# Kernel optimization log

Hardware: AMD Instinct MI355X
Metric: run time of the kernel (lower is better)

The kernel has to match this reference:

```python
import jax, jax.numpy as jnp
import numpy as np

B, T, D = 8, 4096, 1024


def setup_inputs() -> dict:
    key = jax.random.key(0)
    k1, k2 = jax.random.split(key)
    x = jax.random.normal(k1, (B, T, D), dtype=jnp.float32)
    lengths = jax.random.randint(k2, (B,), 0, T, dtype=jnp.int64)
    return {"x": x, "lengths": lengths}


def reference(x, lengths):
    # x: [B, T, D]; lengths: [B]
    # Original torch code materializes a [B,T,T,D] tensor via
    # (tril * pairwise_padding_mask)[..., None] * gelu(x)[:, None] and sums over
    # the source axis. Algebraically:
    #   out[b,i] = x[b,i] + m[b,i] * sum_{j<=i} m[b,j] * gelu(x[b,j])
    # where m[b,t] = (t < lengths[b]). This is a masked causal prefix sum.
    t = x.shape[1]
    valid = (jnp.arange(t)[None, :] < lengths[:, None]).astype(x.dtype)  # [B,T]
    g = jax.nn.gelu(x, approximate=False) * valid[:, :, None]           # [B,T,D]
    prefix = jnp.cumsum(g, axis=1)                                      # [B,T,D]
    return x + valid[:, :, None] * prefix
```

## Files before the change

### kernel.cpp

```cpp
#include <hip/hip_runtime.h>
#include <math.h>

#define BB 8
#define TT 4096
#define DD 1024
#define NC 256
#define CT (TT / NC)
#define D4 (DD / 4)

typedef float vfloat4 __attribute__((ext_vector_type(4)));

__device__ __forceinline__ float gelu_exact(float v) {
    return 0.5f * v * (1.0f + erff(v * 0.70710678118654752f));
}

__device__ __forceinline__ void gelu_acc(float4& s, const float4 v) {
    s.x += gelu_exact(v.x);
    s.y += gelu_exact(v.y);
    s.z += gelu_exact(v.z);
    s.w += gelu_exact(v.w);
}

__global__ __launch_bounds__(256)
void k_partial(const float* __restrict__ x, const int* __restrict__ lengths,
               float* __restrict__ ws) {
    const int c  = blockIdx.x;
    const int b  = blockIdx.y;
    const int d4 = threadIdx.x;
    const int len = lengths[b];
    const int t0 = c * CT;
    if (t0 >= len) return;
    const int t1 = min(t0 + CT, len);

    const float4* __restrict__ xp = (const float4*)(x + (size_t)b * TT * DD);
    float4 s = make_float4(0.f, 0.f, 0.f, 0.f);
    #pragma unroll 4
    for (int t = t0; t < t1; ++t) {
        float4 v = xp[(size_t)t * D4 + d4];
        gelu_acc(s, v);
    }
    ((float4*)ws)[((size_t)b * NC + c) * D4 + d4] = s;
}

__global__ __launch_bounds__(256)
void k_apply(const float* __restrict__ x, const int* __restrict__ lengths,
             const float* __restrict__ ws, float* __restrict__ out) {
    const int c  = blockIdx.x;
    const int b  = blockIdx.y;
    const int d4 = threadIdx.x;
    const int len = lengths[b];
    const int t0 = c * CT;
    const int tv = min(t0 + CT, len);

    const float4* __restrict__ xp = (const float4*)(x + (size_t)b * TT * DD);
    vfloat4* __restrict__ op = (vfloat4*)(out + (size_t)b * TT * DD);

    int t = t0;
    if (t0 < len) {
        float4 p0 = make_float4(0.f, 0.f, 0.f, 0.f);
        float4 p1 = make_float4(0.f, 0.f, 0.f, 0.f);
        const float4* __restrict__ aggp =
            (const float4*)ws + (size_t)b * NC * D4 + d4;
        int cc = 0;
        #pragma unroll 4
        for (; cc + 1 < c; cc += 2) {
            float4 a0 = aggp[(size_t)cc * D4];
            float4 a1 = aggp[(size_t)(cc + 1) * D4];
            p0.x += a0.x; p0.y += a0.y; p0.z += a0.z; p0.w += a0.w;
            p1.x += a1.x; p1.y += a1.y; p1.z += a1.z; p1.w += a1.w;
        }
        if (cc < c) {
            float4 a0 = aggp[(size_t)cc * D4];
            p0.x += a0.x; p0.y += a0.y; p0.z += a0.z; p0.w += a0.w;
        }
        float4 pre = make_float4(p0.x + p1.x, p0.y + p1.y,
                                 p0.z + p1.z, p0.w + p1.w);

        #pragma unroll 4
        for (; t < tv; ++t) {
            float4 v = xp[(size_t)t * D4 + d4];
            gelu_acc(pre, v);
            vfloat4 o = {v.x + pre.x, v.y + pre.y, v.z + pre.z, v.w + pre.w};
            __builtin_nontemporal_store(o, &op[(size_t)t * D4 + d4]);
        }
    }
    #pragma unroll 4
    for (; t < t0 + CT; ++t) {
        float4 v = xp[(size_t)t * D4 + d4];
        vfloat4 o = {v.x, v.y, v.z, v.w};
        __builtin_nontemporal_store(o, &op[(size_t)t * D4 + d4]);
    }
}

extern "C" void kernel_launch(void* const* d_in, const int* in_sizes, int n_in,
                              void* d_out, int out_size, void* d_ws, size_t ws_size,
                              hipStream_t stream) {
    const float* x       = (const float*)d_in[0];
    const int*   lengths = (const int*)d_in[1];
    float*       out     = (float*)d_out;
    float*       ws      = (float*)d_ws;

    dim3 blk(256, 1, 1);
    dim3 g1(NC, BB, 1);
    hipLaunchKernelGGL(k_partial, g1, blk, 0, stream, x, lengths, ws);
    hipLaunchKernelGGL(k_apply,   g1, blk, 0, stream, x, lengths, ws, out);
}
```

Measured before the change: 267.2 us.

## Add hierarchical super-chunk prefix pass to cut per-block aggregate summation

Adds a middle kernel that sums chunk aggregates into super-chunk prefixes, one for every 16 chunks. The apply kernel then starts from the stored super-chunk prefix and adds at most 15 chunk aggregates, instead of re-summing up to 255 for each block. This removes quadratic re-reading of the workspace aggregates. The partial kernel now writes zero aggregates for chunks past the length, so the new prefixes stay correct. In exchange it adds a third kernel launch and one more dependency between stages.

```diff
diff --git a/kernel.cpp b/kernel.cpp
--- a/kernel.cpp
+++ b/kernel.cpp
@@ -7,6 +7,11 @@
 #define NC 256
 #define CT (TT / NC)
 #define D4 (DD / 4)
+#define SCW 16
+#define SC (NC / SCW)
+
+#define AGG_OFF 0
+#define PFX_OFF (BB * NC * DD)
 
 typedef float vfloat4 __attribute__((ext_vector_type(4)));
 
@@ -21,6 +26,10 @@
     s.w += gelu_exact(v.w);
 }
 
+__device__ __forceinline__ void f4_acc(float4& s, const float4 a) {
+    s.x += a.x; s.y += a.y; s.z += a.z; s.w += a.w;
+}
+
 __global__ __launch_bounds__(256)
 void k_partial(const float* __restrict__ x, const int* __restrict__ lengths,
                float* __restrict__ ws) {
@@ -29,7 +38,6 @@
     const int d4 = threadIdx.x;
     const int len = lengths[b];
     const int t0 = c * CT;
-    if (t0 >= len) return;
     const int t1 = min(t0 + CT, len);
 
     const float4* __restrict__ xp = (const float4*)(x + (size_t)b * TT * DD);
@@ -39,7 +47,31 @@
         float4 v = xp[(size_t)t * D4 + d4];
         gelu_acc(s, v);
     }
-    ((float4*)ws)[((size_t)b * NC + c) * D4 + d4] = s;
+    ((float4*)(ws + AGG_OFF))[((size_t)b * NC + c) * D4 + d4] = s;
+}
+
+__global__ __launch_bounds__(256)
+void k_sprefix(float* __restrict__ ws) {
+    const int s  = blockIdx.x;
+    const int b  = blockIdx.y;
+    const int d4 = threadIdx.x;
+    const int n  = s * SCW;
+
+    const float4* __restrict__ aggp =
+        (const float4*)(ws + AGG_OFF) + (size_t)b * NC * D4 + d4;
+    float4 p0 = make_float4(0.f, 0.f, 0.f, 0.f);
+    float4 p1 = make_float4(0.f, 0.f, 0.f, 0.f);
+    int cc = 0;
+    #pragma unroll 4
+    for (; cc + 1 < n; cc += 2) {
+        float4 a0 = aggp[(size_t)cc * D4];
+        float4 a1 = aggp[(size_t)(cc + 1) * D4];
+        f4_acc(p0, a0);
+        f4_acc(p1, a1);
+    }
+    if (cc < n) f4_acc(p0, aggp[(size_t)cc * D4]);
+    f4_acc(p0, p1);
+    ((float4*)(ws + PFX_OFF))[((size_t)b * SC + s) * D4 + d4] = p0;
 }
 
 __global__ __launch_bounds__(256)
@@ -57,24 +89,23 @@
 
     int t = t0;
     if (t0 < len) {
-        float4 p0 = make_float4(0.f, 0.f, 0.f, 0.f);
+        const int sc = c / SCW;
+        float4 pre =
+            ((const float4*)(ws + PFX_OFF))[((size_t)b * SC + sc) * D4 + d4];
+
+        const float4* __restrict__ aggp =
+            (const float4*)(ws + AGG_OFF) + (size_t)b * NC * D4 + d4;
         float4 p1 = make_float4(0.f, 0.f, 0.f, 0.f);
-        const float4* __restrict__ aggp =
-            (const float4*)ws + (size_t)b * NC * D4 + d4;
-        int cc = 0;
+        int cc = sc * SCW;
         #pragma unroll 4
         for (; cc + 1 < c; cc += 2) {
             float4 a0 = aggp[(size_t)cc * D4];
             float4 a1 = aggp[(size_t)(cc + 1) * D4];
-            p0.x += a0.x; p0.y += a0.y; p0.z += a0.z; p0.w += a0.w;
-            p1.x += a1.x; p1.y += a1.y; p1.z += a1.z; p1.w += a1.w;
+            f4_acc(pre, a0);
+            f4_acc(p1, a1);
         }
-        if (cc < c) {
-            float4 a0 = aggp[(size_t)cc * D4];
-            p0.x += a0.x; p0.y += a0.y; p0.z += a0.z; p0.w += a0.w;
-        }
-        float4 pre = make_float4(p0.x + p1.x, p0.y + p1.y,
-                                 p0.z + p1.z, p0.w + p1.w);
+        if (cc < c) f4_acc(pre, aggp[(size_t)cc * D4]);
+        f4_acc(pre, p1);
 
         #pragma unroll 4
         for (; t < tv; ++t) {
@@ -103,5 +134,9 @@
     dim3 blk(256, 1, 1);
     dim3 g1(NC, BB, 1);
     hipLaunchKernelGGL(k_partial, g1, blk, 0, stream, x, lengths, ws);
-    hipLaunchKernelGGL(k_apply,   g1, blk, 0, stream, x, lengths, ws, out);
+
+    dim3 g15(SC, BB, 1);
+    hipLaunchKernelGGL(k_sprefix, g15, blk, 0, stream, ws);
+
+    hipLaunchKernelGGL(k_apply, g1, blk, 0, stream, x, lengths, ws, out);
 }
```

After: 275.2 us. +3.0%, slower.

## Fuse partial and apply kernels into one pass with decoupled chunk flags

Applied to the files above, without the earlier changes.

Merges the two-kernel chunked prefix scan into a single kernel. Each block takes a chunk index from an atomic ticket, computes its chunk's GELU sum, publishes it with a release flag, then spin-waits until all earlier chunks of its batch are flagged before summing their aggregates and writing output. This removes the second kernel launch and the extra pass between launches, and the chunk's x rows may still be in cache when re-read. In exchange it adds a memset of the control area, atomics and spin-waiting, and blocks whose predecessors are slow will stall.

```diff
diff --git a/kernel.cpp b/kernel.cpp
--- a/kernel.cpp
+++ b/kernel.cpp
@@ -7,6 +7,9 @@
 #define NC 256
 #define CT (TT / NC)
 #define D4 (DD / 4)
+
+#define AGG_OFF 0
+#define CTL_OFF (BB * NC * DD)
 
 typedef float vfloat4 __attribute__((ext_vector_type(4)));
 
@@ -21,60 +24,83 @@
     s.w += gelu_exact(v.w);
 }
 
-__global__ __launch_bounds__(256)
-void k_partial(const float* __restrict__ x, const int* __restrict__ lengths,
-               float* __restrict__ ws) {
-    const int c  = blockIdx.x;
-    const int b  = blockIdx.y;
-    const int d4 = threadIdx.x;
-    const int len = lengths[b];
-    const int t0 = c * CT;
-    if (t0 >= len) return;
-    const int t1 = min(t0 + CT, len);
-
-    const float4* __restrict__ xp = (const float4*)(x + (size_t)b * TT * DD);
-    float4 s = make_float4(0.f, 0.f, 0.f, 0.f);
-    #pragma unroll 4
-    for (int t = t0; t < t1; ++t) {
-        float4 v = xp[(size_t)t * D4 + d4];
-        gelu_acc(s, v);
-    }
-    ((float4*)ws)[((size_t)b * NC + c) * D4 + d4] = s;
+__device__ __forceinline__ void f4_acc(float4& s, const float4 a) {
+    s.x += a.x; s.y += a.y; s.z += a.z; s.w += a.w;
 }
 
 __global__ __launch_bounds__(256)
-void k_apply(const float* __restrict__ x, const int* __restrict__ lengths,
-             const float* __restrict__ ws, float* __restrict__ out) {
-    const int c  = blockIdx.x;
-    const int b  = blockIdx.y;
-    const int d4 = threadIdx.x;
+void k_onepass(const float* __restrict__ x, const int* __restrict__ lengths,
+               float* __restrict__ ws, float* __restrict__ out) {
+    float* agg    = ws + AGG_OFF;
+    int*   flags  = (int*)(ws + CTL_OFF);
+    int*   ticket = flags + BB * NC;
+
+    __shared__ int s_tk;
+    __shared__ int s_nr;
+    if (threadIdx.x == 0)
+        s_tk = __hip_atomic_fetch_add(ticket, 1, __ATOMIC_RELAXED,
+                                      __HIP_MEMORY_SCOPE_AGENT);
+    __syncthreads();
+    const int tk  = s_tk;
+    const int b   = tk >> 8;
+    const int c   = tk & (NC - 1);
+    const int d4  = threadIdx.x;
     const int len = lengths[b];
-    const int t0 = c * CT;
-    const int tv = min(t0 + CT, len);
+    const int t0  = c * CT;
+    const int tv  = min(t0 + CT, len);
 
     const float4* __restrict__ xp = (const float4*)(x + (size_t)b * TT * DD);
     vfloat4* __restrict__ op = (vfloat4*)(out + (size_t)b * TT * DD);
 
     int t = t0;
     if (t0 < len) {
-        float4 p0 = make_float4(0.f, 0.f, 0.f, 0.f);
-        float4 p1 = make_float4(0.f, 0.f, 0.f, 0.f);
-        const float4* __restrict__ aggp =
-            (const float4*)ws + (size_t)b * NC * D4 + d4;
-        int cc = 0;
+        float4 s = make_float4(0.f, 0.f, 0.f, 0.f);
         #pragma unroll 4
-        for (; cc + 1 < c; cc += 2) {
-            float4 a0 = aggp[(size_t)cc * D4];
-            float4 a1 = aggp[(size_t)(cc + 1) * D4];
-            p0.x += a0.x; p0.y += a0.y; p0.z += a0.z; p0.w += a0.w;
-            p1.x += a1.x; p1.y += a1.y; p1.z += a1.z; p1.w += a1.w;
+        for (int tt = t0; tt < tv; ++tt) {
+            float4 v = xp[(size_t)tt * D4 + d4];
+            gelu_acc(s, v);
         }
-        if (cc < c) {
-            float4 a0 = aggp[(size_t)cc * D4];
-            p0.x += a0.x; p0.y += a0.y; p0.z += a0.z; p0.w += a0.w;
+        ((float4*)agg)[(size_t)tk * D4 + d4] = s;
+
+        __threadfence();
+        __syncthreads();
+        if (threadIdx.x == 0)
+            __hip_atomic_store(&flags[tk], 1, __ATOMIC_RELEASE,
+                               __HIP_MEMORY_SCOPE_AGENT);
+
+        float4 pre = make_float4(0.f, 0.f, 0.f, 0.f);
+        if (c > 0) {
+            for (;;) {
+                if (threadIdx.x == 0) s_nr = 0;
+                __syncthreads();
+                bool ok = true;
+                if ((int)threadIdx.x < c) {
+                    int f = __hip_atomic_load(&flags[(b << 8) + threadIdx.x],
+                                              __ATOMIC_ACQUIRE,
+                                              __HIP_MEMORY_SCOPE_AGENT);
+                    ok = (f != 0);
+                }
+                if (!ok) s_nr = 1;
+                __syncthreads();
+                if (s_nr == 0) break;
+                __builtin_amdgcn_s_sleep(2);
+            }
+            __threadfence();
+
+            const float4* __restrict__ aggp =
+                (const float4*)agg + (size_t)(b << 8) * D4 + d4;
+            float4 p1 = make_float4(0.f, 0.f, 0.f, 0.f);
+            int cc = 0;
+            #pragma unroll 4
+            for (; cc + 1 < c; cc += 2) {
+                float4 a0 = aggp[(size_t)cc * D4];
+                float4 a1 = aggp[(size_t)(cc + 1) * D4];
+                f4_acc(pre, a0);
+                f4_acc(p1, a1);
+            }
+            if (cc < c) f4_acc(pre, aggp[(size_t)cc * D4]);
+            f4_acc(pre, p1);
         }
-        float4 pre = make_float4(p0.x + p1.x, p0.y + p1.y,
-                                 p0.z + p1.z, p0.w + p1.w);
 
         #pragma unroll 4
         for (; t < tv; ++t) {
@@ -100,8 +126,10 @@
     float*       out     = (float*)d_out;
     float*       ws      = (float*)d_ws;
 
+    hipMemsetAsync((char*)ws + (size_t)CTL_OFF * sizeof(float), 0,
+                   (BB * NC + 1) * sizeof(int), stream);
+
     dim3 blk(256, 1, 1);
-    dim3 g1(NC, BB, 1);
-    hipLaunchKernelGGL(k_partial, g1, blk, 0, stream, x, lengths, ws);
-    hipLaunchKernelGGL(k_apply,   g1, blk, 0, stream, x, lengths, ws, out);
+    dim3 grd(NC * BB, 1, 1);
+    hipLaunchKernelGGL(k_onepass, grd, blk, 0, stream, x, lengths, ws, out);
 }
```

Result: slower. 697.9 us (+161.2%).
